# Kernel tuning notes

Hardware: AMD Instinct MI355X
Metric: run time of the kernel (lower is better)

Reference implementation:

```python
import jax, jax.numpy as jnp
import numpy as np

H_SIZE = 64  # height_pad == width_pad == 64 (power of 2, no padding needed)


def _hadamard(n):
    H = np.array([[1.0]], dtype=np.float32)
    while H.shape[0] < n:
        H = np.block([[H, H], [H, -H]])
    return jnp.asarray(H)


def setup_inputs() -> dict:
    key = jax.random.key(0)
    k1, k2, k3, k4 = jax.random.split(key, 4)
    B, C_in, C_out, P = 32, 256, 256, 2
    x = jax.random.normal(k1, (B, C_in, H_SIZE, H_SIZE), dtype=jnp.float32)
    v = jax.random.uniform(k2, (P, H_SIZE, H_SIZE), dtype=jnp.float32)
    W = jax.random.normal(k3, (P, C_out, C_in), dtype=jnp.float32) * (1.0 / np.sqrt(C_in))
    T = jax.random.uniform(k4, (P, H_SIZE, H_SIZE), dtype=jnp.float32) * 0.1
    return {"x": x, "v": v, "W": W, "T": T}


def reference(x, v, W, T):
    n = H_SIZE
    H = _hadamard(n)  # symmetric, H @ H = n * I
    # 2D WHT: apply along width then height
    f1 = jnp.einsum('bchw,wk->bchk', x, H)
    f2 = jnp.einsum('bchw,hk->bckw', f1, H)
    # per-pod: scale, 1x1 conv, soft-threshold
    f3 = v[:, None, None, :, :] * f2[None]                 # (p,b,c,h,w)
    f4 = jnp.einsum('poc,pbchw->pbohw', W, f3)             # 1x1 conv, no bias
    f5 = jnp.sign(f4) * jnp.maximum(jnp.abs(f4) - T[:, None, None, :, :], 0.0)
    f6 = f5.sum(axis=0)                                     # sum over pods
    # inverse 2D WHT (H^{-1} = H / n)
    f7 = jnp.einsum('bchw,wk->bchk', f6, H) / n
    f8 = jnp.einsum('bchw,hk->bckw', f7, H) / n
    return f8 + x  # residual
```

## Files before the change

### kernel.cpp

```cpp
#include <hip/hip_runtime.h>
#include <stdint.h>


typedef __attribute__((ext_vector_type(4))) float f32x4_t;
typedef __attribute__((ext_vector_type(8))) __bf16 bf16x8_t;
typedef __attribute__((ext_vector_type(8))) unsigned short u16x8_t;
typedef __attribute__((ext_vector_type(4))) unsigned short u16x4_t;

__device__ __forceinline__ float bf2f(unsigned short u) {
  union { unsigned int i; float f; } x; x.i = ((unsigned int)u) << 16; return x.f;
}
__device__ __forceinline__ unsigned short f2bf(float f) {
  union { float f; unsigned int i; } x; x.f = f;
  unsigned int i = x.i;
  return (unsigned short)((i + 0x7FFFu + ((i >> 16) & 1u)) >> 16);
}
__device__ __forceinline__ unsigned short f2bf_t(float f) {
  union { float f; unsigned int i; } x; x.f = f;
  return (unsigned short)(x.i >> 16);
}
__device__ __forceinline__ size_t Faddr(size_t f) {
  return ((f >> 12) << 13) + 4096 + (f & 4095);
}

__global__ __launch_bounds__(512) void k_fwd(const float* __restrict__ x,
                                             unsigned short* __restrict__ obuf) {
  __shared__ unsigned short smem[36864];
  int tid = threadIdx.x;
  int lane = tid & 63, wave = tid >> 6;
  int quad = lane >> 4, l15 = lane & 15;
  int cg = blockIdx.x, b = blockIdx.y;
  size_t img = (size_t)b * 256 + cg * 8 + wave;
  unsigned short* T1t = smem + wave * 4608;

  const float* xim = x + img * 4096;
#pragma unroll
  for (int l = 0; l < 16; l++) {
    int e = (l * 64 + lane) * 4;
    f32x4_t sv = *(const f32x4_t*)(xim + e);
    u16x4_t u;
#pragma unroll
    for (int j = 0; j < 4; j++) u[j] = f2bf_t(sv[j]);
    int row = e >> 6, col = e & 63;
    *(u16x4_t*)&T1t[row * 72 + col] = u;
  }

  bf16x8_t hf[2][4];
#pragma unroll
  for (int kc = 0; kc < 2; kc++)
#pragma unroll
    for (int t = 0; t < 4; t++) {
      bf16x8_t h;
#pragma unroll
      for (int j = 0; j < 8; j++) {
        int k = kc * 32 + quad * 8 + j, n = t * 16 + l15;
        h[j] = (__builtin_popcount(k & n) & 1) ? (__bf16)-1.0f : (__bf16)1.0f;
      }
      hf[kc][t] = h;
    }

  bf16x8_t xa[4][2];
#pragma unroll
  for (int mt = 0; mt < 4; mt++)
#pragma unroll
    for (int kc = 0; kc < 2; kc++)
      xa[mt][kc] = *(const bf16x8_t*)&T1t[(mt * 16 + l15) * 72 + kc * 32 + quad * 8];

#pragma unroll
  for (int nt = 0; nt < 4; nt++) {
    f32x4_t a1c[4];
#pragma unroll
    for (int mt = 0; mt < 4; mt++) a1c[mt] = (f32x4_t){0.f, 0.f, 0.f, 0.f};
#pragma unroll
    for (int kc = 0; kc < 2; kc++)
#pragma unroll
      for (int mt = 0; mt < 4; mt++)
        a1c[mt] = __builtin_amdgcn_mfma_f32_16x16x32_bf16(xa[mt][kc], hf[kc][nt], a1c[mt], 0, 0, 0);
#pragma unroll
    for (int mt = 0; mt < 4; mt++) {
      u16x4_t t4;
#pragma unroll
      for (int r = 0; r < 4; r++) t4[r] = f2bf_t(a1c[mt][r]);
      *(u16x4_t*)&T1t[(nt * 16 + l15) * 72 + mt * 16 + quad * 4] = t4;
    }
  }

  f32x4_t acc[4][4];
#pragma unroll
  for (int mt = 0; mt < 4; mt++)
#pragma unroll
    for (int nt = 0; nt < 4; nt++) acc[mt][nt] = (f32x4_t){0.f, 0.f, 0.f, 0.f};
#pragma unroll
  for (int kc = 0; kc < 2; kc++)
#pragma unroll
    for (int nt = 0; nt < 4; nt++) {
      bf16x8_t bfr = *(bf16x8_t*)&T1t[(nt * 16 + l15) * 72 + kc * 32 + quad * 8];
#pragma unroll
      for (int mt = 0; mt < 4; mt++)
        acc[mt][nt] = __builtin_amdgcn_mfma_f32_16x16x32_bf16(hf[kc][mt], bfr, acc[mt][nt], 0, 0, 0);
    }

  __syncthreads();
#pragma unroll
  for (int mt = 0; mt < 4; mt++)
#pragma unroll
    for (int nt = 0; nt < 4; nt++)
#pragma unroll
      for (int r = 0; r < 4; r++) {
        int pos = (mt * 16 + quad * 4 + r) * 64 + nt * 16 + l15;
        smem[pos * 8 + wave] = f2bf(acc[mt][nt][r]);
      }
  __syncthreads();
  size_t fbase = ((size_t)b * 32 + cg) * 4096;
#pragma unroll
  for (int i = 0; i < 8; i++) {
    int pos = i * 512 + tid;
    u16x8_t vch = *(u16x8_t*)&smem[pos * 8];
    *(u16x8_t*)(obuf + Faddr((fbase + pos) * 8)) = vch;
  }
}

__global__ __launch_bounds__(256) void k_gemm(const float* __restrict__ Wf,
                                              const float* __restrict__ vv,
                                              const float* __restrict__ TT,
                                              unsigned short* __restrict__ obuf) {
  __shared__ unsigned short smem2[16384];
  unsigned short* Alds = smem2;
  unsigned short* Blds = smem2 + 8192;
  int tid = threadIdx.x;
  int lane = tid & 63, wave = tid >> 6;
  int quad = lane >> 4, l15 = lane & 15;
  int wm = wave & 1, wn = wave >> 1;
  int n0 = blockIdx.x * 128;
  int m0 = blockIdx.y * 128;
  int b  = blockIdx.z;

  f32x4_t acc[4][4];
#pragma unroll
  for (int mt = 0; mt < 4; mt++)
#pragma unroll
    for (int nt = 0; nt < 4; nt++) acc[mt][nt] = (f32x4_t){0.f, 0.f, 0.f, 0.f};

  for (int ks = 0; ks < 4; ++ks) {
    int k0 = ks * 64;
    u16x8_t va[4], vb[4];
#pragma unroll
    for (int i = 0; i < 4; i++) {
      int idx = i * 256 + tid;
      {
        int r = idx >> 3, cch = idx & 7;
        int gch = cch ^ (r & 7);
        int m = m0 + r;
        const float* wp = Wf + ((m & 1) << 16) + ((m >> 1) << 8) + k0 + gch * 8;
        f32x4_t w0 = *(const f32x4_t*)wp;
        f32x4_t w1 = *(const f32x4_t*)(wp + 4);
        u16x8_t u;
#pragma unroll
        for (int j = 0; j < 4; j++) { u[j] = f2bf_t(w0[j]); u[4 + j] = f2bf_t(w1[j]); }
        va[i] = u;
      }
      {
        int r = idx & 127, cch = idx >> 7;
        size_t f = (((size_t)b * 32 + ks * 8 + cch) * 4096 + n0 + r) * 8;
        vb[i] = *(const u16x8_t*)(obuf + Faddr(f));
      }
    }
#pragma unroll
    for (int i = 0; i < 4; i++) {
      int idx = i * 256 + tid;
      *(u16x8_t*)&Alds[idx * 8] = va[i];
      int r = idx & 127, cch = idx >> 7;
      int s = cch ^ (r & 7);
      *(u16x8_t*)&Blds[r * 64 + s * 8] = vb[i];
    }
    __syncthreads();

#pragma unroll
    for (int kk = 0; kk < 2; ++kk) {
      bf16x8_t af[4], bfr[4];
#pragma unroll
      for (int mt = 0; mt < 4; mt++) {
        int row = wm * 64 + mt * 16 + l15;
        int ch = (kk * 4 + quad) ^ (row & 7);
        af[mt] = *(const bf16x8_t*)&Alds[row * 64 + ch * 8];
      }
#pragma unroll
      for (int nt = 0; nt < 4; nt++) {
        int row = wn * 64 + nt * 16 + l15;
        int ch = (kk * 4 + quad) ^ (row & 7);
        bfr[nt] = *(const bf16x8_t*)&Blds[row * 64 + ch * 8];
      }
#pragma unroll
      for (int mt = 0; mt < 4; mt++)
#pragma unroll
        for (int nt = 0; nt < 4; nt++)
          acc[mt][nt] = __builtin_amdgcn_mfma_f32_16x16x32_bf16(af[mt], bfr[nt], acc[mt][nt], 0, 0, 0);
    }
    __syncthreads();
  }

#pragma unroll
  for (int nt = 0; nt < 4; nt++) {
    int posl = wn * 64 + nt * 16 + l15;
    int pos = n0 + posl;
    float v0 = vv[pos], v1 = vv[4096 + pos];
    float t0 = TT[pos], t1 = TT[4096 + pos];
#pragma unroll
    for (int mt = 0; mt < 4; mt++)
#pragma unroll
      for (int rp = 0; rp < 2; rp++) {
        int ol = wm * 32 + mt * 8 + quad * 2 + rp;
        float z0 = acc[mt][nt][rp * 2 + 0] * v0;
        float z1 = acc[mt][nt][rp * 2 + 1] * v1;
        float s0 = copysignf(fmaxf(fabsf(z0) - t0, 0.f), z0);
        float s1 = copysignf(fmaxf(fabsf(z1) - t1, 0.f), z1);
        smem2[ol * 136 + posl] = f2bf(s0 + s1);
      }
  }
  __syncthreads();
  int o0 = m0 >> 1;
#pragma unroll
  for (int i = 0; i < 4; i++) {
    int ci = i * 256 + tid;
    int row = ci >> 4, cc = ci & 15;
    u16x8_t vch = *(u16x8_t*)&smem2[row * 136 + cc * 8];
    size_t img = (size_t)b * 256 + o0 + row;
    *(u16x8_t*)(obuf + img * 8192 + n0 + cc * 8) = vch;
  }
}

__global__ __launch_bounds__(256) void k_inv(const float* __restrict__ x,
                                             unsigned short* __restrict__ obuf) {
  __shared__ unsigned short smem[18432];
  int tid = threadIdx.x;
  int lane = tid & 63, wave = tid >> 6;
  int quad = lane >> 4, l15 = lane & 15;
  size_t img = (size_t)blockIdx.x * 4 + wave;
  unsigned short* T1t = smem + wave * 4608;

#pragma unroll
  for (int l = 0; l < 8; l++) {
    int e = (l * 64 + lane) * 8;
    u16x8_t sv = *(const u16x8_t*)(obuf + img * 8192 + e);
    int row = e >> 6, col = e & 63;
    *(u16x8_t*)&T1t[row * 72 + col] = sv;
  }

  bf16x8_t hf[2][4];
#pragma unroll
  for (int kc = 0; kc < 2; kc++)
#pragma unroll
    for (int t = 0; t < 4; t++) {
      bf16x8_t h;
#pragma unroll
      for (int j = 0; j < 8; j++) {
        int k = kc * 32 + quad * 8 + j, n = t * 16 + l15;
        h[j] = (__builtin_popcount(k & n) & 1) ? (__bf16)-1.0f : (__bf16)1.0f;
      }
      hf[kc][t] = h;
    }

  bf16x8_t fa[4][2];
#pragma unroll
  for (int mt = 0; mt < 4; mt++)
#pragma unroll
    for (int kc = 0; kc < 2; kc++)
      fa[mt][kc] = *(const bf16x8_t*)&T1t[(mt * 16 + l15) * 72 + kc * 32 + quad * 8];

#pragma unroll
  for (int nt = 0; nt < 4; nt++) {
    f32x4_t a1c[4];
#pragma unroll
    for (int mt = 0; mt < 4; mt++) a1c[mt] = (f32x4_t){0.f, 0.f, 0.f, 0.f};
#pragma unroll
    for (int kc = 0; kc < 2; kc++)
#pragma unroll
      for (int mt = 0; mt < 4; mt++)
        a1c[mt] = __builtin_amdgcn_mfma_f32_16x16x32_bf16(fa[mt][kc], hf[kc][nt], a1c[mt], 0, 0, 0);
#pragma unroll
    for (int mt = 0; mt < 4; mt++) {
      u16x4_t t4;
#pragma unroll
      for (int r = 0; r < 4; r++) t4[r] = f2bf_t(a1c[mt][r]);
      *(u16x4_t*)&T1t[(nt * 16 + l15) * 72 + mt * 16 + quad * 4] = t4;
    }
  }

  f32x4_t acc[4][4];
#pragma unroll
  for (int mt = 0; mt < 4; mt++)
#pragma unroll
    for (int nt = 0; nt < 4; nt++) acc[mt][nt] = (f32x4_t){0.f, 0.f, 0.f, 0.f};
#pragma unroll
  for (int kc = 0; kc < 2; kc++)
#pragma unroll
    for (int nt = 0; nt < 4; nt++) {
      bf16x8_t bfr = *(bf16x8_t*)&T1t[(nt * 16 + l15) * 72 + kc * 32 + quad * 8];
#pragma unroll
      for (int mt = 0; mt < 4; mt++)
        acc[mt][nt] = __builtin_amdgcn_mfma_f32_16x16x32_bf16(hf[kc][mt], bfr, acc[mt][nt], 0, 0, 0);
    }

  const float sc = 1.0f / 4096.0f;
#pragma unroll
  for (int mt = 0; mt < 4; mt++)
#pragma unroll
    for (int nt = 0; nt < 4; nt++)
#pragma unroll
      for (int r = 0; r < 4; r++)
        T1t[(mt * 16 + quad * 4 + r) * 72 + nt * 16 + l15] = f2bf(acc[mt][nt][r] * sc);

  float* outf = (float*)obuf;
  const float* xim = x + img * 4096;
#pragma unroll
  for (int l = 0; l < 8; l++) {
    int e = (l * 64 + lane) * 8;
    int row = e >> 6, col = e & 63;
    u16x8_t tv = *(u16x8_t*)&T1t[row * 72 + col];
    f32x4_t x0 = *(const f32x4_t*)(xim + e);
    f32x4_t x1 = *(const f32x4_t*)(xim + e + 4);
    f32x4_t o0, o1;
#pragma unroll
    for (int j = 0; j < 4; j++) { o0[j] = bf2f(tv[j]) + x0[j]; o1[j] = bf2f(tv[4 + j]) + x1[j]; }
    *(f32x4_t*)(outf + img * 4096 + e) = o0;
    *(f32x4_t*)(outf + img * 4096 + e + 4) = o1;
  }
}

extern "C" void kernel_launch(void* const* d_in, const int* in_sizes, int n_in,
                              void* d_out, int out_size, void* d_ws, size_t ws_size,
                              hipStream_t stream) {
  const float* x = (const float*)d_in[0];
  const float* v = (const float*)d_in[1];
  const float* W = (const float*)d_in[2];
  const float* T = (const float*)d_in[3];
  unsigned short* obuf = (unsigned short*)d_out;
  (void)d_ws; (void)ws_size; (void)in_sizes; (void)n_in; (void)out_size;

  k_fwd<<<dim3(32, 32), 512, 0, stream>>>(x, obuf);
  k_gemm<<<dim3(32, 4, 32), 256, 0, stream>>>(W, v, T, obuf);
  k_inv<<<2048, 256, 0, stream>>>(x, obuf);
}
```

Measured before the change: 337.4 us.

## Double-buffer B tiles via global_load_lds and prefetch A into registers

The GEMM main loop now streams the B tile straight from global memory into LDS with global_load_lds into a double buffer, and prefetches the next A tile into registers while the current tile's MFMAs run. The LDS layout becomes channel-major (ch*1024 + row*8) with no XOR swizzle, so fragment reads are contiguous 16-byte loads. This is meant to overlap global-load latency with compute and drop the register round trip for B. In exchange LDS use grows by half, and no explicit vmcnt wait is visible before the async LDS data is consumed beyond __syncthreads.

```diff
diff --git a/kernel.cpp b/kernel.cpp
--- a/kernel.cpp
+++ b/kernel.cpp
@@ -124,9 +124,8 @@
                                               const float* __restrict__ vv,
                                               const float* __restrict__ TT,
                                               unsigned short* __restrict__ obuf) {
-  __shared__ unsigned short smem2[16384];
+  __shared__ unsigned short smem2[24576];
   unsigned short* Alds = smem2;
-  unsigned short* Blds = smem2 + 8192;
   int tid = threadIdx.x;
   int lane = tid & 63, wave = tid >> 6;
   int quad = lane >> 4, l15 = lane & 15;
@@ -141,55 +140,66 @@
 #pragma unroll
     for (int nt = 0; nt < 4; nt++) acc[mt][nt] = (f32x4_t){0.f, 0.f, 0.f, 0.f};
 
-  for (int ks = 0; ks < 4; ++ks) {
-    int k0 = ks * 64;
-    u16x8_t va[4], vb[4];
+  auto issueB = [&](int ks, int buf) {
+    unsigned short* Bl = smem2 + 8192 + buf * 8192;
 #pragma unroll
     for (int i = 0; i < 4; i++) {
       int idx = i * 256 + tid;
-      {
-        int r = idx >> 3, cch = idx & 7;
-        int gch = cch ^ (r & 7);
-        int m = m0 + r;
-        const float* wp = Wf + ((m & 1) << 16) + ((m >> 1) << 8) + k0 + gch * 8;
-        f32x4_t w0 = *(const f32x4_t*)wp;
-        f32x4_t w1 = *(const f32x4_t*)(wp + 4);
-        u16x8_t u;
-#pragma unroll
-        for (int j = 0; j < 4; j++) { u[j] = f2bf_t(w0[j]); u[4 + j] = f2bf_t(w1[j]); }
-        va[i] = u;
-      }
-      {
-        int r = idx & 127, cch = idx >> 7;
-        size_t f = (((size_t)b * 32 + ks * 8 + cch) * 4096 + n0 + r) * 8;
-        vb[i] = *(const u16x8_t*)(obuf + Faddr(f));
-      }
-    }
+      int r = idx & 127, cch = idx >> 7;
+      size_t f = (((size_t)b * 32 + ks * 8 + cch) * 4096 + n0 + r) * 8;
+      const unsigned short* src = obuf + Faddr(f);
+      __builtin_amdgcn_global_load_lds(
+          (const __attribute__((address_space(1))) void*)src,
+          (__attribute__((address_space(3))) void*)(Bl + idx * 8), 16, 0, 0);
+    }
+  };
+  auto loadA = [&](int ks, f32x4_t (&ar)[4][2]) {
+    int k0 = ks * 64;
 #pragma unroll
     for (int i = 0; i < 4; i++) {
       int idx = i * 256 + tid;
-      *(u16x8_t*)&Alds[idx * 8] = va[i];
-      int r = idx & 127, cch = idx >> 7;
-      int s = cch ^ (r & 7);
-      *(u16x8_t*)&Blds[r * 64 + s * 8] = vb[i];
-    }
-    __syncthreads();
-
+      int r = idx >> 3, cch = idx & 7;
+      int m = m0 + r;
+      const float* wp = Wf + ((m & 1) << 16) + ((m >> 1) << 8) + k0 + cch * 8;
+      ar[i][0] = *(const f32x4_t*)wp;
+      ar[i][1] = *(const f32x4_t*)(wp + 4);
+    }
+  };
+  auto writeA = [&](f32x4_t (&ar)[4][2]) {
+#pragma unroll
+    for (int i = 0; i < 4; i++) {
+      int idx = i * 256 + tid;
+      int r = idx >> 3, cch = idx & 7;
+      u16x8_t u;
+#pragma unroll
+      for (int j = 0; j < 4; j++) { u[j] = f2bf_t(ar[i][0][j]); u[4 + j] = f2bf_t(ar[i][1][j]); }
+      *(u16x8_t*)&Alds[cch * 1024 + r * 8] = u;
+    }
+  };
+
+  f32x4_t areg[4][2];
+  issueB(0, 0);
+  loadA(0, areg);
+  writeA(areg);
+  __syncthreads();
+
+  int kbuf = 0;
+  for (int ks = 0; ks < 4; ++ks) {
+    if (ks < 3) {
+      issueB(ks + 1, kbuf ^ 1);
+      loadA(ks + 1, areg);
+    }
+    unsigned short* Bl = smem2 + 8192 + kbuf * 8192;
 #pragma unroll
     for (int kk = 0; kk < 2; ++kk) {
+      int ch = kk * 4 + quad;
       bf16x8_t af[4], bfr[4];
 #pragma unroll
-      for (int mt = 0; mt < 4; mt++) {
-        int row = wm * 64 + mt * 16 + l15;
-        int ch = (kk * 4 + quad) ^ (row & 7);
-        af[mt] = *(const bf16x8_t*)&Alds[row * 64 + ch * 8];
-      }
-#pragma unroll
-      for (int nt = 0; nt < 4; nt++) {
-        int row = wn * 64 + nt * 16 + l15;
-        int ch = (kk * 4 + quad) ^ (row & 7);
-        bfr[nt] = *(const bf16x8_t*)&Blds[row * 64 + ch * 8];
-      }
+      for (int mt = 0; mt < 4; mt++)
+        af[mt] = *(const bf16x8_t*)&Alds[ch * 1024 + (wm * 64 + mt * 16 + l15) * 8];
+#pragma unroll
+      for (int nt = 0; nt < 4; nt++)
+        bfr[nt] = *(const bf16x8_t*)&Bl[ch * 1024 + (wn * 64 + nt * 16 + l15) * 8];
 #pragma unroll
       for (int mt = 0; mt < 4; mt++)
 #pragma unroll
@@ -197,6 +207,11 @@
           acc[mt][nt] = __builtin_amdgcn_mfma_f32_16x16x32_bf16(af[mt], bfr[nt], acc[mt][nt], 0, 0, 0);
     }
     __syncthreads();
+    if (ks < 3) {
+      writeA(areg);
+      __syncthreads();
+    }
+    kbuf ^= 1;
   }
 
 #pragma unroll
```

Result: slower. 353.1 us (+4.6%).
